# Performance work log

Hardware: AMD Instinct MI355X
Metric: run time of the kernel (lower is better)

## Reference

```python
import jax, jax.numpy as jnp
import numpy as np

N = 10000
E = 160000
F_IN = 2000
HID = 128
NC = 5


def setup_inputs() -> dict:
    key = jax.random.key(0)
    ks = jax.random.split(key, 16)
    s = 0.05
    nrm = lambda k, shape: jax.random.normal(k, shape, jnp.float32) * s
    return {
        "x": jax.random.normal(ks[0], (N, F_IN), jnp.float32),
        "edge_index": jax.random.randint(ks[1], (2, E), 0, N),
        # GATConv 1: in=F_IN, out=HID, heads=6, concat=False
        "W_gat1": nrm(ks[2], (F_IN, 6 * HID)), "a_src1": nrm(ks[3], (6, HID)),
        "a_dst1": nrm(ks[4], (6, HID)), "b_gat1": jnp.zeros(HID, jnp.float32),
        # GCNConv 1
        "W_gcn1": nrm(ks[5], (HID, HID)), "b_gcn1": jnp.zeros(HID, jnp.float32),
        # GATConv 2: heads=4
        "W_gat2": nrm(ks[6], (HID, 4 * HID)), "a_src2": nrm(ks[7], (4, HID)),
        "a_dst2": nrm(ks[8], (4, HID)), "b_gat2": jnp.zeros(HID, jnp.float32),
        # GCNConv 2: out=HID//2
        "W_gcn2": nrm(ks[9], (HID, HID // 2)), "b_gcn2": jnp.zeros(HID // 2, jnp.float32),
        # skip projection / fusion
        "W_skip": nrm(ks[10], (F_IN, HID // 2)), "b_skip": jnp.zeros(HID // 2, jnp.float32),
        "W_fuse": nrm(ks[11], (HID + HID // 2, HID // 2)), "b_fuse": jnp.zeros(HID // 2, jnp.float32),
        # classifier MLP
        "W_c1": nrm(ks[12], (HID // 2, HID // 4)), "b_c1": jnp.zeros(HID // 4, jnp.float32),
        "W_c2": nrm(ks[13], (HID // 4, HID // 8)), "b_c2": jnp.zeros(HID // 8, jnp.float32),
        "W_c3": nrm(ks[14], (HID // 8, NC)), "b_c3": jnp.zeros(NC, jnp.float32),
        # LayerNorms
        "g1": jnp.ones(HID, jnp.float32), "be1": jnp.zeros(HID, jnp.float32),
        "g2": jnp.ones(HID, jnp.float32), "be2": jnp.zeros(HID, jnp.float32),
        "g3": jnp.ones(HID // 2, jnp.float32), "be3": jnp.zeros(HID // 2, jnp.float32),
    }


def layer_norm(x, g, b, eps=1e-5):
    mu = jnp.mean(x, axis=-1, keepdims=True)
    var = jnp.var(x, axis=-1, keepdims=True)
    return (x - mu) * jax.lax.rsqrt(var + eps) * g + b


def gat_conv(x, src, dst, W, a_src, a_dst, b, n):
    # PyG GATConv with concat=False (head-mean). Eval mode -> no attn dropout.
    H, C = a_src.shape
    h = (x @ W).reshape(-1, H, C)                      # [N,H,C]
    alpha = (h * a_src).sum(-1)[src] + (h * a_dst).sum(-1)[dst]  # [E,H]
    alpha = jax.nn.leaky_relu(alpha, 0.2)
    m = jax.ops.segment_max(alpha, dst, num_segments=n)
    e = jnp.exp(alpha - m[dst])
    w = e / jax.ops.segment_sum(e, dst, num_segments=n)[dst]     # segment softmax over incoming edges
    out = jax.ops.segment_sum(h[src] * w[:, :, None], dst, num_segments=n)  # [N,H,C]
    return out.mean(axis=1) + b


def gcn_conv(x, src, dst, W, b, n):
    deg = jax.ops.segment_sum(jnp.ones_like(dst, x.dtype), dst, num_segments=n)
    dinv = jnp.where(deg > 0, deg ** -0.5, 0.0)
    msg = (x @ W)[src] * (dinv[src] * dinv[dst])[:, None]
    return jax.ops.segment_sum(msg, dst, num_segments=n) + b


def reference(x, edge_index, W_gat1, a_src1, a_dst1, b_gat1, W_gcn1, b_gcn1,
              W_gat2, a_src2, a_dst2, b_gat2, W_gcn2, b_gcn2,
              W_skip, b_skip, W_fuse, b_fuse, W_c1, b_c1, W_c2, b_c2, W_c3, b_c3,
              g1, be1, g2, be2, g3, be3):
    n = x.shape[0]
    loop = jnp.arange(n, dtype=edge_index.dtype)
    src = jnp.concatenate([edge_index[0], loop])  # add_self_loops
    dst = jnp.concatenate([edge_index[1], loop])

    x1_gat = jax.nn.relu(layer_norm(gat_conv(x, src, dst, W_gat1, a_src1, a_dst1, b_gat1, n), g1, be1))
    x1_gcn = jax.nn.relu(gcn_conv(x1_gat, src, dst, W_gcn1, b_gcn1, n))
    x2_gat = jax.nn.relu(layer_norm(gat_conv(x1_gcn, src, dst, W_gat2, a_src2, a_dst2, b_gat2, n), g2, be2))
    x2_gcn = jax.nn.relu(gcn_conv(x2_gat, src, dst, W_gcn2, b_gcn2, n))

    skip = jax.nn.relu(x @ W_skip + b_skip)
    fused = jax.nn.relu(jnp.concatenate([x1_gcn, x2_gcn], axis=1) @ W_fuse + b_fuse)
    final = layer_norm(fused + skip, g3, be3)

    h = jax.nn.relu(final @ W_c1 + b_c1)
    h = jax.nn.relu(h @ W_c2 + b_c2)
    return h @ W_c3 + b_c3
```

## Files before the change

### kernel.cpp

```cpp
#include <hip/hip_runtime.h>
#include <cstdint>
#include <cstddef>

#define NN 10000
#define NE 160000
#define ET (NE + NN)
#define FIN 2000
#define MPAD 10112
#define KPAD 2048
#define NPAD 896

typedef __bf16 bf16x8 __attribute__((ext_vector_type(8)));
typedef __bf16 bf16x4 __attribute__((ext_vector_type(4)));
typedef float  f32x4  __attribute__((ext_vector_type(4)));

#define GLL(src, dst) __builtin_amdgcn_global_load_lds( \
    (const __attribute__((address_space(1))) void*)(src), \
    (__attribute__((address_space(3))) void*)(dst), 16, 0, 0)

__device__ __forceinline__ void edge_sd(const int* ei, int e, int& s, int& d) {
    if (e < NE) { s = ei[e]; d = ei[NE + e]; }
    else        { s = e - NE; d = e - NE; }
}

__global__ void scan_kernel(const int* deg, int* rowstart, float* dinv) {
    __shared__ int partial[256];
    const int T = 256;
    int chunk = (NN + T - 1) / T;
    int t = threadIdx.x;
    int begin = t * chunk;
    int end = begin + chunk; if (end > NN) end = NN;
    int s = 0;
    for (int i = begin; i < end && i >= begin; i++) s += deg[i];
    partial[t] = s;
    __syncthreads();
    if (t == 0) {
        int run = 0;
        for (int i = 0; i < T; i++) { int v = partial[i]; partial[i] = run; run += v; }
    }
    __syncthreads();
    int run = partial[t];
    for (int i = begin; i < end && i >= begin; i++) {
        rowstart[i] = run; run += deg[i];
        int dg = deg[i];
        dinv[i] = dg > 0 ? rsqrtf((float)dg) : 0.f;
    }
    if (end == NN && begin <= NN) rowstart[NN] = run;
}

__global__ void scatter_kernel(const int* ei, const int* rowstart, int* cursor,
                               int* csr_src) {
    int e = blockIdx.x * blockDim.x + threadIdx.x;
    if (e >= ET) return;
    int s, d; edge_sd(ei, e, s, d);
    int pos = atomicAdd(&cursor[d], 1);
    csr_src[rowstart[d] + pos] = s;
}

#define NBX (158 * 32)
#define NW1 (NPAD * KPAD / 8)
#define NWT (NW1 + 512 * 128 / 8)
#define NWT2 (NWT + 2048 + 1024)
#define WBLK ((NWT2 + 255) / 256)
#define EB 665
__global__ void conv_kernel(const float* __restrict__ x, __bf16* __restrict__ xb,
                            const float* __restrict__ Wg, const float* __restrict__ Ws,
                            const float* __restrict__ W2,
                            const float* __restrict__ Wg1, const float* __restrict__ Wg2,
                            __bf16* __restrict__ wt, __bf16* __restrict__ w2t,
                            __bf16* __restrict__ wgcn1s, __bf16* __restrict__ wgcn2s,
                            const int* __restrict__ ei, int* __restrict__ deg) {
    __shared__ __bf16 slab[4096];
    int bid = blockIdx.x;
    int tid = threadIdx.x;
    if (bid < NBX) {
        int rt = bid >> 5, ks = bid & 31;
        int r = tid >> 2;
        int row = rt * 64 + r;
        int c0 = (tid & 3) * 16;
        int kbase = ks * 64;
#pragma unroll
        for (int j = 0; j < 4; j++) {
            int kl = c0 + j * 4;
            int k = kbase + kl;
            bf16x4 o;
            if (row < NN && k + 3 < FIN) {
                float4 v = *(const float4*)(x + (size_t)row * FIN + k);
                o[0] = (__bf16)v.x; o[1] = (__bf16)v.y;
                o[2] = (__bf16)v.z; o[3] = (__bf16)v.w;
            } else {
                o[0] = o[1] = o[2] = o[3] = (__bf16)0.f;
            }
            int p = kl >> 3, off = kl & 7;
            *(bf16x4*)(slab + (p * 64 + r) * 8 + off) = o;
        }
        __syncthreads();
        size_t base = (size_t)(rt * 32 + ks) * 512;
#pragma unroll
        for (int i = 0; i < 2; i++) {
            int c = i * 256 + tid;
            *(bf16x8*)(xb + (base + c) * 8) = *(const bf16x8*)(slab + c * 8);
        }
    } else if (bid < NBX + WBLK) {
        int g = (bid - NBX) * 256 + tid;
        if (g < NW1) {
            int r = g & 127, p = (g >> 7) & 7, ks = (g >> 10) & 31, ct = g >> 15;
            int n = ct * 128 + r;
            int k0 = ks * 64 + p * 8;
            bf16x8 o;
#pragma unroll
            for (int j = 0; j < 8; j++) {
                int k = k0 + j;
                float v = 0.f;
                if (k < FIN) {
                    if (n < 768)      v = Wg[(size_t)k * 768 + n];
                    else if (n < 832) v = Ws[(size_t)k * 64 + (n - 768)];
                }
                o[j] = (__bf16)v;
            }
            *(bf16x8*)(wt + (size_t)g * 8) = o;
        } else if (g < NWT) {
            int g2 = g - NW1;
            int c = g2 & 2047;
            int ct = g2 >> 11;
            int p = c >> 7, r = c & 127;
            int n = ct * 128 + r;
            int k0 = p * 8;
            bf16x8 o;
#pragma unroll
            for (int j = 0; j < 8; j++)
                o[j] = (__bf16)W2[(size_t)(k0 + j) * 512 + n];
            *(bf16x8*)(w2t + (size_t)g2 * 8) = o;
        } else if (g < NWT + 2048) {
            int g3 = g - NWT;
            int p = g3 >> 7, r = g3 & 127;
            bf16x8 o;
#pragma unroll
            for (int j = 0; j < 8; j++)
                o[j] = (__bf16)Wg1[(size_t)(p * 8 + j) * 128 + r];
            *(bf16x8*)(wgcn1s + (size_t)g3 * 8) = o;
        } else if (g < NWT2) {
            int g4 = g - NWT - 2048;
            int p = g4 >> 6, r = g4 & 63;
            bf16x8 o;
#pragma unroll
            for (int j = 0; j < 8; j++)
                o[j] = (__bf16)Wg2[(size_t)(p * 8 + j) * 64 + r];
            *(bf16x8*)(wgcn2s + (size_t)g4 * 8) = o;
        }
    } else {
        int e = (bid - NBX - WBLK) * 256 + tid;
        if (e < ET) {
            int s, d; edge_sd(ei, e, s, d);
            atomicAdd(&deg[d], 1);
        }
    }
}

__global__ __launch_bounds__(256)
void mfma_gemm1_kernel(const __bf16* __restrict__ xb, const __bf16* __restrict__ wt,
                       const float* __restrict__ a_src1, const float* __restrict__ a_dst1,
                       __bf16* __restrict__ h1b, float* __restrict__ skippre,
                       float* __restrict__ asrc, float* __restrict__ adst) {
    __shared__ __bf16 As[4096];
    __shared__ __bf16 Bs[8192];
    __shared__ float sA[64], sD[64];
    __shared__ float asd[256];
    int b = blockIdx.x;
    int xcd = b & 7, j = b >> 3;
    int jq = j / 7;
    int rt = xcd + 8 * jq;
    int ct = j - 7 * jq;
    if (rt >= MPAD / 64) return;
    const int bi = rt * 64;
    const int bn = ct * 128;

    const int tid = threadIdx.x;
    const int lane = tid & 63;
    const int w = tid >> 6;
    const int wm = w >> 1, wn = w & 1;
    const int q = lane >> 4, m16 = lane & 15;

    if (tid < 64) { sA[tid] = 0.f; sD[tid] = 0.f; }
    if (ct < 6) {
        if (tid < 128) asd[tid] = a_src1[ct * 128 + tid];
        else           asd[tid] = a_dst1[ct * 128 + (tid - 128)];
    }

    f32x4 acc[2][4] = {};

    for (int ks = 0; ks < KPAD / 64; ks++) {
        const size_t slabA = (size_t)(rt * 32 + ks) * 512;
        const size_t slabB = (size_t)(ct * 32 + ks) * 1024;
#pragma unroll
        for (int i = 0; i < 2; i++) {
            int seg = i * 4 + w;
            GLL(xb + (slabA + seg * 64 + lane) * 8, As + seg * 512);
        }
#pragma unroll
        for (int i = 0; i < 4; i++) {
            int seg = i * 4 + w;
            GLL(wt + (slabB + seg * 64 + lane) * 8, Bs + seg * 512);
        }
        __syncthreads();

#pragma unroll
        for (int kk = 0; kk < 2; kk++) {
            const int pb = kk * 4 + q;
            bf16x8 af[2], bfr[4];
#pragma unroll
            for (int mt = 0; mt < 2; mt++)
                af[mt] = *(const bf16x8*)(As + (pb * 64 + wm * 32 + mt * 16 + m16) * 8);
#pragma unroll
            for (int nt = 0; nt < 4; nt++)
                bfr[nt] = *(const bf16x8*)(Bs + (pb * 128 + wn * 64 + nt * 16 + m16) * 8);
#pragma unroll
            for (int mt = 0; mt < 2; mt++)
#pragma unroll
                for (int nt = 0; nt < 4; nt++)
                    acc[mt][nt] = __builtin_amdgcn_mfma_f32_16x16x32_bf16(af[mt], bfr[nt], acc[mt][nt], 0, 0, 0);
        }
        __syncthreads();
    }

#pragma unroll
    for (int mt = 0; mt < 2; mt++) {
#pragma unroll
        for (int r = 0; r < 4; r++) {
            int rowl = wm * 32 + mt * 16 + q * 4 + r;
            int row = bi + rowl;
            float ps = 0.f, pd = 0.f;
#pragma unroll
            for (int nt = 0; nt < 4; nt++) {
                int coll = wn * 64 + nt * 16 + m16;
                int col = bn + coll;
                float v = acc[mt][nt][r];
                if (ct < 6) { ps += v * asd[coll]; pd += v * asd[128 + coll]; }
                if (row < NN) {
                    if (col < 768)      h1b[(size_t)row * 768 + col] = (__bf16)v;
                    else if (col < 832) skippre[(size_t)row * 64 + (col - 768)] = v;
                }
            }
            if (ct < 6) {
#pragma unroll
                for (int off = 1; off < 16; off <<= 1) {
                    ps += __shfl_xor(ps, off);
                    pd += __shfl_xor(pd, off);
                }
                if (m16 == 0) { atomicAdd(&sA[rowl], ps); atomicAdd(&sD[rowl], pd); }
            }
        }
    }
    if (ct < 6) {
        __syncthreads();
        if (tid < 64) {
            int row = bi + tid;
            if (row < NN) { asrc[row * 6 + ct] = sA[tid]; adst[row * 6 + ct] = sD[tid]; }
        }
    }
}

__global__ __launch_bounds__(256)
void mfma_gemm2_kernel(const __bf16* __restrict__ A, const __bf16* __restrict__ B,
                       const float* __restrict__ a_src2, const float* __restrict__ a_dst2,
                       __bf16* __restrict__ h2b,
                       float* __restrict__ asrc, float* __restrict__ adst) {
    __shared__ __bf16 As[4096];
    __shared__ __bf16 Bs[8192];
    __shared__ float sA[64], sD[64];
    __shared__ float asd[256];
    const int rt = blockIdx.y, ct = blockIdx.x;
    const int bi = rt * 64, bn = ct * 128;
    const int tid = threadIdx.x, lane = tid & 63, w = tid >> 6;
    const int wm = w >> 1, wn = w & 1;
    const int q = lane >> 4, m16 = lane & 15;

    if (tid < 64) { sA[tid] = 0.f; sD[tid] = 0.f; }
    if (tid < 128) asd[tid] = a_src2[ct * 128 + tid];
    else           asd[tid] = a_dst2[ct * 128 + (tid - 128)];

    f32x4 acc[2][4] = {};

    for (int ks = 0; ks < 2; ks++) {
        const size_t slabA = (size_t)rt * 1024 + ks * 512;
        const size_t slabB = (size_t)ct * 2048 + ks * 1024;
#pragma unroll
        for (int i = 0; i < 2; i++) {
            int seg = i * 4 + w;
            GLL(A + (slabA + seg * 64 + lane) * 8, As + seg * 512);
        }
#pragma unroll
        for (int i = 0; i < 4; i++) {
            int seg = i * 4 + w;
            GLL(B + (slabB + seg * 64 + lane) * 8, Bs + seg * 512);
        }
        __syncthreads();

#pragma unroll
        for (int kk = 0; kk < 2; kk++) {
            const int pb = kk * 4 + q;
            bf16x8 af[2], bfr[4];
#pragma unroll
            for (int mt = 0; mt < 2; mt++)
                af[mt] = *(const bf16x8*)(As + (pb * 64 + wm * 32 + mt * 16 + m16) * 8);
#pragma unroll
            for (int nt = 0; nt < 4; nt++)
                bfr[nt] = *(const bf16x8*)(Bs + (pb * 128 + wn * 64 + nt * 16 + m16) * 8);
#pragma unroll
            for (int mt = 0; mt < 2; mt++)
#pragma unroll
                for (int nt = 0; nt < 4; nt++)
                    acc[mt][nt] = __builtin_amdgcn_mfma_f32_16x16x32_bf16(af[mt], bfr[nt], acc[mt][nt], 0, 0, 0);
        }
        __syncthreads();
    }

#pragma unroll
    for (int mt = 0; mt < 2; mt++) {
#pragma unroll
        for (int r = 0; r < 4; r++) {
            int rowl = wm * 32 + mt * 16 + q * 4 + r;
            int row = bi + rowl;
            float ps = 0.f, pd = 0.f;
#pragma unroll
            for (int nt = 0; nt < 4; nt++) {
                int coll = wn * 64 + nt * 16 + m16;
                float v = acc[mt][nt][r];
                ps += v * asd[coll]; pd += v * asd[128 + coll];
                if (row < NN) h2b[(size_t)row * 512 + bn + coll] = (__bf16)v;
            }
#pragma unroll
            for (int off = 1; off < 16; off <<= 1) {
                ps += __shfl_xor(ps, off);
                pd += __shfl_xor(pd, off);
            }
            if (m16 == 0) { atomicAdd(&sA[rowl], ps); atomicAdd(&sD[rowl], pd); }
        }
    }
    __syncthreads();
    if (tid < 64) {
        int row = bi + tid;
        if (row < NN) { asrc[row * 4 + ct] = sA[tid]; adst[row * 4 + ct] = sD[tid]; }
    }
}

template<int NT>
__global__ __launch_bounds__(256)
void mfma_gcn_kernel(const __bf16* __restrict__ A, const __bf16* __restrict__ B,
                     __bf16* __restrict__ Cb) {
    __shared__ __bf16 As[4096];
    __shared__ __bf16 Bs[NT * 64];
    const int rt = blockIdx.x;
    const int bi = rt * 64;
    const int tid = threadIdx.x, lane = tid & 63, w = tid >> 6;
    const int q = lane >> 4, m16 = lane & 15;
    constexpr int MT = (NT == 128) ? 2 : 1;
    constexpr int MSPAN = (NT == 128) ? 32 : 16;
    const int wm = (NT == 128) ? (w >> 1) : w;
    const int wn = (NT == 128) ? (w & 1) : 0;

    f32x4 acc[MT][4] = {};

    for (int ks = 0; ks < 2; ks++) {
        const size_t slabA = (size_t)rt * 1024 + ks * 512;
        const size_t slabB = (size_t)ks * (NT * 8);
#pragma unroll
        for (int i = 0; i < 2; i++) {
            int seg = i * 4 + w;
            GLL(A + (slabA + seg * 64 + lane) * 8, As + seg * 512);
        }
#pragma unroll
        for (int i = 0; i < NT / 32; i++) {
            int seg = i * 4 + w;
            GLL(B + (slabB + (size_t)seg * 64 + lane) * 8, Bs + seg * 512);
        }
        __syncthreads();

#pragma unroll
        for (int kk = 0; kk < 2; kk++) {
            const int pb = kk * 4 + q;
            bf16x8 af[MT], bfr[4];
#pragma unroll
            for (int mt = 0; mt < MT; mt++)
                af[mt] = *(const bf16x8*)(As + (pb * 64 + wm * MSPAN + mt * 16 + m16) * 8);
#pragma unroll
            for (int nt = 0; nt < 4; nt++)
                bfr[nt] = *(const bf16x8*)(Bs + (pb * NT + wn * 64 + nt * 16 + m16) * 8);
#pragma unroll
            for (int mt = 0; mt < MT; mt++)
#pragma unroll
                for (int nt = 0; nt < 4; nt++)
                    acc[mt][nt] = __builtin_amdgcn_mfma_f32_16x16x32_bf16(af[mt], bfr[nt], acc[mt][nt], 0, 0, 0);
        }
        __syncthreads();
    }

#pragma unroll
    for (int mt = 0; mt < MT; mt++) {
#pragma unroll
        for (int r = 0; r < 4; r++) {
            int row = bi + wm * MSPAN + mt * 16 + q * 4 + r;
            if (row >= NN) continue;
#pragma unroll
            for (int nt = 0; nt < 4; nt++) {
                int col = wn * 64 + nt * 16 + m16;
                Cb[(size_t)row * NT + col] = (__bf16)acc[mt][nt][r];
            }
        }
    }
}

template<int H>
__global__ void gat_agg_kernel(const __bf16* __restrict__ hb,
                               const float* __restrict__ asrc,
                               const float* __restrict__ adst,
                               const int* __restrict__ rowstart,
                               const int* __restrict__ csr_src,
                               const float* __restrict__ bias,
                               const float* __restrict__ gamma,
                               const float* __restrict__ beta,
                               __bf16* __restrict__ outs) {
    constexpr int CH = H * 128;
    constexpr int CAP = 128;
    int n = blockIdx.x;
    int t = threadIdx.x;
    int w = t >> 6, l = t & 63;
    __shared__ float invden[H];
    __shared__ float denw[4][H];
    __shared__ int   srcs[CAP];
    __shared__ float evs[CAP * H];
    __shared__ float sm[4 * CH];
    __shared__ float red[8];

    int s0 = rowstart[n];
    int deg = rowstart[n + 1] - s0;
    float adst_n = (l < H) ? adst[n * H + l] : 0.f;

    float dloc = 0.f;
    for (int idx = w; idx < deg; idx += 4) {
        int src = csr_src[s0 + idx];
        if (idx < CAP && l == 0) srcs[idx] = src;
        if (l < H) {
            float al = asrc[src * H + l] + adst_n;
            al = al >= 0.f ? al : 0.2f * al;
            float ev = __expf(al);
            dloc += ev;
            if (idx < CAP) evs[idx * H + l] = ev;
        }
    }
    if (l < H) denw[w][l] = dloc;
    __syncthreads();
    if (t < H) invden[t] = 1.f / (denw[0][t] + denw[1][t] + denw[2][t] + denw[3][t]);
    __syncthreads();

    constexpr int NA = (H == 6) ? 12 : 8;
    float acc[NA] = {};
    const int h0 = l >> 4;
    const int h1i = 4 + (l >> 5);
    int degc = deg < CAP ? deg : CAP;
    int idx = w;
    for (; idx + 4 < degc; idx += 8) {
        int src0 = srcs[idx], src1 = srcs[idx + 4];
        float w00 = evs[idx * H + h0];
        float w10 = evs[(idx + 4) * H + h0];
        const __bf16* hp0 = hb + (size_t)src0 * CH;
        const __bf16* hp1 = hb + (size_t)src1 * CH;
        bf16x8 g00 = *(const bf16x8*)(hp0 + l * 8);
        bf16x8 g10 = *(const bf16x8*)(hp1 + l * 8);
#pragma unroll
        for (int jj = 0; jj < 8; jj++)
            acc[jj] += (float)g00[jj] * w00 + (float)g10[jj] * w10;
        if (H == 6) {
            float w01 = evs[idx * H + h1i];
            float w11 = evs[(idx + 4) * H + h1i];
            bf16x4 g01 = *(const bf16x4*)(hp0 + 512 + l * 4);
            bf16x4 g11 = *(const bf16x4*)(hp1 + 512 + l * 4);
#pragma unroll
            for (int jj = 0; jj < 4; jj++)
                acc[8 + jj] += (float)g01[jj] * w01 + (float)g11[jj] * w11;
        }
    }
    if (idx < degc) {
        int src = srcs[idx];
        float w0 = evs[idx * H + h0];
        const __bf16* hp = hb + (size_t)src * CH;
        bf16x8 hv = *(const bf16x8*)(hp + l * 8);
#pragma unroll
        for (int jj = 0; jj < 8; jj++) acc[jj] += (float)hv[jj] * w0;
        if (H == 6) {
            float w1 = evs[idx * H + h1i];
            bf16x4 hv1 = *(const bf16x4*)(hp + 512 + l * 4);
#pragma unroll
            for (int jj = 0; jj < 4; jj++) acc[8 + jj] += (float)hv1[jj] * w1;
        }
    }
    for (int i2 = CAP + w; i2 < deg; i2 += 4) {
        int src = csr_src[s0 + i2];
        float ev = 0.f;
        if (l < H) {
            float al = asrc[src * H + l] + adst_n;
            al = al >= 0.f ? al : 0.2f * al;
            ev = __expf(al);
        }
        const __bf16* hp = hb + (size_t)src * CH;
        float wgt = __shfl(ev, h0);
        bf16x8 hv = *(const bf16x8*)(hp + l * 8);
#pragma unroll
        for (int jj = 0; jj < 8; jj++) acc[jj] += (float)hv[jj] * wgt;
        if (H == 6) {
            float wg1 = __shfl(ev, h1i);
            bf16x4 hv1 = *(const bf16x4*)(hp + 512 + l * 4);
#pragma unroll
            for (int jj = 0; jj < 4; jj++) acc[8 + jj] += (float)hv1[jj] * wg1;
        }
    }

    *(f32x4*)(sm + w * CH + l * 8)     = *(f32x4*)(acc);
    *(f32x4*)(sm + w * CH + l * 8 + 4) = *(f32x4*)(acc + 4);
    if (H == 6)
        *(f32x4*)(sm + w * CH + 512 + l * 4) = *(f32x4*)(acc + 8);
    __syncthreads();

    float v = 0.f;
    if (t < 128) {
#pragma unroll
        for (int hh = 0; hh < H; hh++) {
            float hsum = 0.f;
#pragma unroll
            for (int ww = 0; ww < 4; ww++) hsum += sm[ww * CH + hh * 128 + t];
            v += hsum * invden[hh];
        }
        v = v * (1.f / H) + bias[t];
    }
    float sv = (t < 128) ? v : 0.f;
    float sq = (t < 128) ? v * v : 0.f;
#pragma unroll
    for (int off = 32; off; off >>= 1) {
        sv += __shfl_down(sv, off);
        sq += __shfl_down(sq, off);
    }
    if ((t & 63) == 0) { red[w * 2] = sv; red[w * 2 + 1] = sq; }
    __syncthreads();
    float tot = red[0] + red[2] + red[4] + red[6];
    float tsq = red[1] + red[3] + red[5] + red[7];
    float mu = tot * (1.f / 128.f);
    float var = tsq * (1.f / 128.f) - mu * mu;
    float r = rsqrtf(var + 1e-5f);
    if (t < 128) {
        float o = fmaxf((v - mu) * r * gamma[t] + beta[t], 0.f);
        int rt2 = n >> 6, rr = n & 63, pp = t >> 3, off2 = t & 7;
        outs[((size_t)(rt2 * 16 + pp) * 64 + rr) * 8 + off2] = (__bf16)o;
    }
}

__global__ void gcn_agg_kernel(const __bf16* __restrict__ y, int C,
                               const float* __restrict__ dinv,
                               const int* __restrict__ rowstart,
                               const int* __restrict__ csr_src,
                               const float* __restrict__ bias,
                               float* __restrict__ out, int ldo, int coloff,
                               __bf16* __restrict__ bout) {
    int n = blockIdx.x;
    int t = threadIdx.x;
    float acc = 0.f;
    int s0 = rowstart[n], s1 = rowstart[n + 1];
    for (int s = s0; s < s1; s++) {
        int src = csr_src[s];
        acc += (float)y[(size_t)src * C + t] * dinv[src];
    }
    float v = fmaxf(acc * dinv[n] + bias[t], 0.f);
    out[(size_t)n * ldo + coloff + t] = v;
    if (bout) {
        int rt = n >> 6, r = n & 63, p = t >> 3, off = t & 7;
        bout[((size_t)(rt * 16 + p) * 64 + r) * 8 + off] = (__bf16)v;
    }
}

__global__ __launch_bounds__(256)
void fuse_final_kernel(const float* __restrict__ cat,
                       const float* __restrict__ skippre,
                       const float* __restrict__ Wf, const float* __restrict__ bfz,
                       const float* __restrict__ b_skip,
                       const float* __restrict__ g3, const float* __restrict__ be3,
                       const float* __restrict__ Wc1, const float* __restrict__ bc1,
                       const float* __restrict__ Wc2, const float* __restrict__ bc2,
                       const float* __restrict__ Wc3, const float* __restrict__ bc3,
                       float* __restrict__ out) {
    __shared__ float WfS[192 * 64];
    __shared__ float catS[4][196];
    __shared__ float fS[4][64], h1S[4][32], h2S[4][16];
    int tid = threadIdx.x;
    int w = tid >> 6, l = tid & 63;
#pragma unroll
    for (int i = 0; i < 12; i++) {
        int idx = (i * 256 + tid) * 4;
        *(f32x4*)(WfS + idx) = *(const f32x4*)(Wf + idx);
    }
    int n = blockIdx.x * 4 + w;
    bool act = n < NN;
    float sk = 0.f;
    if (act) {
        catS[w][l]       = cat[(size_t)n * 192 + l];
        catS[w][64 + l]  = cat[(size_t)n * 192 + 64 + l];
        catS[w][128 + l] = cat[(size_t)n * 192 + 128 + l];
        sk = fmaxf(skippre[(size_t)n * 64 + l] + b_skip[l], 0.f);
    }
    __syncthreads();

    float fu = bfz[l];
#pragma unroll 4
    for (int k = 0; k < 192; k++)
        fu += catS[w][k] * WfS[k * 64 + l];
    float v = fmaxf(fu, 0.f) + sk;

    float sv = v, sq = v * v;
#pragma unroll
    for (int off = 32; off; off >>= 1) {
        sv += __shfl_xor(sv, off);
        sq += __shfl_xor(sq, off);
    }
    float mu = sv * (1.f / 64.f);
    float var = sq * (1.f / 64.f) - mu * mu;
    float r = rsqrtf(var + 1e-5f);
    fS[w][l] = (v - mu) * r * g3[l] + be3[l];
    __syncthreads();
    if (l < 32) {
        float a = bc1[l];
        for (int i = 0; i < 64; i++) a += fS[w][i] * Wc1[i * 32 + l];
        h1S[w][l] = fmaxf(a, 0.f);
    }
    __syncthreads();
    if (l < 16) {
        float a = bc2[l];
        for (int i = 0; i < 32; i++) a += h1S[w][i] * Wc2[i * 16 + l];
        h2S[w][l] = fmaxf(a, 0.f);
    }
    __syncthreads();
    if (l < 5 && act) {
        float a = bc3[l];
        for (int i = 0; i < 16; i++) a += h2S[w][i] * Wc3[i * 5 + l];
        out[(size_t)n * 5 + l] = a;
    }
}

extern "C" void kernel_launch(void* const* d_in, const int* in_sizes, int n_in,
                              void* d_out, int out_size, void* d_ws, size_t ws_size,
                              hipStream_t stream) {
    const float* x      = (const float*)d_in[0];
    const int*   ei     = (const int*)d_in[1];
    const float* W_gat1 = (const float*)d_in[2];
    const float* a_src1 = (const float*)d_in[3];
    const float* a_dst1 = (const float*)d_in[4];
    const float* b_gat1 = (const float*)d_in[5];
    const float* W_gcn1 = (const float*)d_in[6];
    const float* b_gcn1 = (const float*)d_in[7];
    const float* W_gat2 = (const float*)d_in[8];
    const float* a_src2 = (const float*)d_in[9];
    const float* a_dst2 = (const float*)d_in[10];
    const float* b_gat2 = (const float*)d_in[11];
    const float* W_gcn2 = (const float*)d_in[12];
    const float* b_gcn2 = (const float*)d_in[13];
    const float* W_skip = (const float*)d_in[14];
    const float* b_skip = (const float*)d_in[15];
    const float* W_fuse = (const float*)d_in[16];
    const float* b_fuse = (const float*)d_in[17];
    const float* W_c1   = (const float*)d_in[18];
    const float* b_c1   = (const float*)d_in[19];
    const float* W_c2   = (const float*)d_in[20];
    const float* b_c2   = (const float*)d_in[21];
    const float* W_c3   = (const float*)d_in[22];
    const float* b_c3   = (const float*)d_in[23];
    const float* g1     = (const float*)d_in[24];
    const float* be1    = (const float*)d_in[25];
    const float* g2     = (const float*)d_in[26];
    const float* be2    = (const float*)d_in[27];
    const float* g3     = (const float*)d_in[28];
    const float* be3    = (const float*)d_in[29];
    float* out = (float*)d_out;

    char* p = (char*)d_ws;
    auto alloc = [&](size_t bytes) {
        char* r = p; p += (bytes + 255) & ~(size_t)255; return r;
    };
    __bf16* xb      = (__bf16*)alloc((size_t)MPAD * KPAD * 2);
    __bf16* wt      = (__bf16*)alloc((size_t)NPAD * KPAD * 2);
    __bf16* w2t     = (__bf16*)alloc((size_t)512 * 128 * 2);
    __bf16* wgcn1s  = (__bf16*)alloc((size_t)128 * 128 * 2);
    __bf16* wgcn2s  = (__bf16*)alloc((size_t)64 * 128 * 2);
    __bf16* h1b     = (__bf16*)alloc((size_t)NN * 768 * 2);
    __bf16* h2b     = (__bf16*)alloc((size_t)NN * 512 * 2);
    __bf16* ybufb   = (__bf16*)alloc((size_t)NN * 128 * 2);
    __bf16* x1gatb  = (__bf16*)alloc((size_t)3 * MPAD * 128 * 2);
    __bf16* x1gcnb  = x1gatb + (size_t)MPAD * 128;
    __bf16* x2gatb  = x1gcnb + (size_t)MPAD * 128;
    float* asrc     = (float*)alloc((size_t)NN * 6 * 4);
    float* adst     = (float*)alloc((size_t)NN * 6 * 4);
    int*   deg      = (int*)  alloc((size_t)2 * NN * 4);
    int*   cursor   = deg + NN;
    float* dinv     = (float*)alloc((size_t)NN * 4);
    int*   rowst    = (int*)  alloc((size_t)(NN + 1) * 4);
    int*   csrc     = (int*)  alloc((size_t)ET * 4);
    float* cat      = (float*)alloc((size_t)NN * 192 * 4);
    float* skippre  = (float*)alloc((size_t)NN * 64 * 4);

    hipMemsetAsync(deg, 0, (size_t)2 * NN * 4, stream);
    hipMemsetAsync(x1gatb, 0, (size_t)3 * MPAD * 128 * 2, stream);

    conv_kernel<<<NBX + WBLK + EB, 256, 0, stream>>>(
        x, xb, W_gat1, W_skip, W_gat2, W_gcn1, W_gcn2,
        wt, w2t, wgcn1s, wgcn2s, ei, deg);

    scan_kernel   <<<1, 256, 0, stream>>>(deg, rowst, dinv);
    scatter_kernel<<<EB, 256, 0, stream>>>(ei, rowst, cursor, csrc);

    mfma_gemm1_kernel<<<1120, 256, 0, stream>>>(xb, wt, a_src1, a_dst1,
                                                h1b, skippre, asrc, adst);

    gat_agg_kernel<6><<<NN, 256, 0, stream>>>(h1b, asrc, adst, rowst, csrc,
                                              b_gat1, g1, be1, x1gatb);
    mfma_gcn_kernel<128><<<MPAD / 64, 256, 0, stream>>>(x1gatb, wgcn1s, ybufb);
    gcn_agg_kernel<<<NN, 128, 0, stream>>>(ybufb, 128, dinv, rowst, csrc,
                                           b_gcn1, cat, 192, 0, x1gcnb);
    mfma_gemm2_kernel<<<dim3(4, MPAD / 64), 256, 0, stream>>>(
        x1gcnb, w2t, a_src2, a_dst2, h2b, asrc, adst);
    gat_agg_kernel<4><<<NN, 256, 0, stream>>>(h2b, asrc, adst, rowst, csrc,
                                              b_gat2, g2, be2, x2gatb);
    mfma_gcn_kernel<64><<<MPAD / 64, 256, 0, stream>>>(x2gatb, wgcn2s, ybufb);
    gcn_agg_kernel<<<NN, 64, 0, stream>>>(ybufb, 64, dinv, rowst, csrc,
                                          b_gcn2, cat, 192, 128, nullptr);
    fuse_final_kernel<<<(NN + 3) / 4, 256, 0, stream>>>(
        cat, skippre, W_fuse, b_fuse, b_skip, g3, be3,
        W_c1, b_c1, W_c2, b_c2, W_c3, b_c3, out);
}
```

Baseline: 469.1 us.

## Fold CSR scatter into GEMM1 launch, split GCN edges across groups, amortize fuse weights

The CSR scatter kernel is removed and its work runs as extra trailing blocks of the first MFMA GEMM launch, which saves one launch and lets the scatter overlap with the GEMM. The GCN aggregation kernel is templated on channel count and uses 256 threads, so several thread groups split each node's edge list and combine partial sums through shared memory. The fuse/final kernel processes 16 nodes per block instead of 4, so the 48KB fusion weight matrix is loaded into shared memory fewer times. The costs are extra barriers and a shared-memory reduction in the aggregation, and fewer blocks in the fuse kernel.

After: 532.2 us. 13.5% more time.

```diff
diff --git a/kernel.cpp b/kernel.cpp
--- a/kernel.cpp
+++ b/kernel.cpp
@@ -46,15 +46,6 @@
         dinv[i] = dg > 0 ? rsqrtf((float)dg) : 0.f;
     }
     if (end == NN && begin <= NN) rowstart[NN] = run;
-}
-
-__global__ void scatter_kernel(const int* ei, const int* rowstart, int* cursor,
-                               int* csr_src) {
-    int e = blockIdx.x * blockDim.x + threadIdx.x;
-    if (e >= ET) return;
-    int s, d; edge_sd(ei, e, s, d);
-    int pos = atomicAdd(&cursor[d], 1);
-    csr_src[rowstart[d] + pos] = s;
 }
 
 #define NBX (158 * 32)
@@ -157,16 +148,28 @@
     }
 }
 
+#define G1BLK 1120
 __global__ __launch_bounds__(256)
 void mfma_gemm1_kernel(const __bf16* __restrict__ xb, const __bf16* __restrict__ wt,
                        const float* __restrict__ a_src1, const float* __restrict__ a_dst1,
                        __bf16* __restrict__ h1b, float* __restrict__ skippre,
-                       float* __restrict__ asrc, float* __restrict__ adst) {
+                       float* __restrict__ asrc, float* __restrict__ adst,
+                       const int* __restrict__ ei, const int* __restrict__ rowstart,
+                       int* __restrict__ cursor, int* __restrict__ csr_src) {
     __shared__ __bf16 As[4096];
     __shared__ __bf16 Bs[8192];
     __shared__ float sA[64], sD[64];
     __shared__ float asd[256];
     int b = blockIdx.x;
+    if (b >= G1BLK) {
+        int e = (b - G1BLK) * 256 + threadIdx.x;
+        if (e < ET) {
+            int s, d; edge_sd(ei, e, s, d);
+            int pos = atomicAdd(&cursor[d], 1);
+            csr_src[rowstart[d] + pos] = s;
+        }
+        return;
+    }
     int xcd = b & 7, j = b >> 3;
     int jq = j / 7;
     int rt = xcd + 8 * jq;
@@ -553,26 +556,36 @@
     }
 }
 
-__global__ void gcn_agg_kernel(const __bf16* __restrict__ y, int C,
+template<int C>
+__global__ void gcn_agg_kernel(const __bf16* __restrict__ y,
                                const float* __restrict__ dinv,
                                const int* __restrict__ rowstart,
                                const int* __restrict__ csr_src,
                                const float* __restrict__ bias,
                                float* __restrict__ out, int ldo, int coloff,
                                __bf16* __restrict__ bout) {
+    constexpr int G = 256 / C;
     int n = blockIdx.x;
     int t = threadIdx.x;
+    int g = t / C, ch = t % C;
+    __shared__ float part[256];
     float acc = 0.f;
     int s0 = rowstart[n], s1 = rowstart[n + 1];
-    for (int s = s0; s < s1; s++) {
+    for (int s = s0 + g; s < s1; s += G) {
         int src = csr_src[s];
-        acc += (float)y[(size_t)src * C + t] * dinv[src];
-    }
-    float v = fmaxf(acc * dinv[n] + bias[t], 0.f);
-    out[(size_t)n * ldo + coloff + t] = v;
-    if (bout) {
-        int rt = n >> 6, r = n & 63, p = t >> 3, off = t & 7;
-        bout[((size_t)(rt * 16 + p) * 64 + r) * 8 + off] = (__bf16)v;
+        acc += (float)y[(size_t)src * C + ch] * dinv[src];
+    }
+    part[t] = acc;
+    __syncthreads();
+    if (g == 0) {
+#pragma unroll
+        for (int i = 1; i < G; i++) acc += part[i * C + ch];
+        float v = fmaxf(acc * dinv[n] + bias[ch], 0.f);
+        out[(size_t)n * ldo + coloff + ch] = v;
+        if (bout) {
+            int rt = n >> 6, r = n & 63, p = ch >> 3, off = ch & 7;
+            bout[((size_t)(rt * 16 + p) * 64 + r) * 8 + off] = (__bf16)v;
+        }
     }
 }
 
@@ -596,50 +609,55 @@
         int idx = (i * 256 + tid) * 4;
         *(f32x4*)(WfS + idx) = *(const f32x4*)(Wf + idx);
     }
-    int n = blockIdx.x * 4 + w;
-    bool act = n < NN;
-    float sk = 0.f;
-    if (act) {
-        catS[w][l]       = cat[(size_t)n * 192 + l];
-        catS[w][64 + l]  = cat[(size_t)n * 192 + 64 + l];
-        catS[w][128 + l] = cat[(size_t)n * 192 + 128 + l];
-        sk = fmaxf(skippre[(size_t)n * 64 + l] + b_skip[l], 0.f);
-    }
-    __syncthreads();
-
-    float fu = bfz[l];
+    __syncthreads();
+
+    for (int it = 0; it < 4; it++) {
+        int n = blockIdx.x * 16 + it * 4 + w;
+        bool act = n < NN;
+        float sk = 0.f;
+        if (act) {
+            catS[w][l]       = cat[(size_t)n * 192 + l];
+            catS[w][64 + l]  = cat[(size_t)n * 192 + 64 + l];
+            catS[w][128 + l] = cat[(size_t)n * 192 + 128 + l];
+            sk = fmaxf(skippre[(size_t)n * 64 + l] + b_skip[l], 0.f);
+        }
+        __syncthreads();
+
+        float fu = bfz[l];
 #pragma unroll 4
-    for (int k = 0; k < 192; k++)
-        fu += catS[w][k] * WfS[k * 64 + l];
-    float v = fmaxf(fu, 0.f) + sk;
-
-    float sv = v, sq = v * v;
-#pragma unroll
-    for (int off = 32; off; off >>= 1) {
-        sv += __shfl_xor(sv, off);
-        sq += __shfl_xor(sq, off);
-    }
-    float mu = sv * (1.f / 64.f);
-    float var = sq * (1.f / 64.f) - mu * mu;
-    float r = rsqrtf(var + 1e-5f);
-    fS[w][l] = (v - mu) * r * g3[l] + be3[l];
-    __syncthreads();
-    if (l < 32) {
-        float a = bc1[l];
-        for (int i = 0; i < 64; i++) a += fS[w][i] * Wc1[i * 32 + l];
-        h1S[w][l] = fmaxf(a, 0.f);
-    }
-    __syncthreads();
-    if (l < 16) {
-        float a = bc2[l];
-        for (int i = 0; i < 32; i++) a += h1S[w][i] * Wc2[i * 16 + l];
-        h2S[w][l] = fmaxf(a, 0.f);
-    }
-    __syncthreads();
-    if (l < 5 && act) {
-        float a = bc3[l];
-        for (int i = 0; i < 16; i++) a += h2S[w][i] * Wc3[i * 5 + l];
-        out[(size_t)n * 5 + l] = a;
+        for (int k = 0; k < 192; k++)
+            fu += catS[w][k] * WfS[k * 64 + l];
+        float v = fmaxf(fu, 0.f) + sk;
+
+        float sv = v, sq = v * v;
+#pragma unroll
+        for (int off = 32; off; off >>= 1) {
+            sv += __shfl_xor(sv, off);
+            sq += __shfl_xor(sq, off);
+        }
+        float mu = sv * (1.f / 64.f);
+        float var = sq * (1.f / 64.f) - mu * mu;
+        float r = rsqrtf(var + 1e-5f);
+        fS[w][l] = (v - mu) * r * g3[l] + be3[l];
+        __syncthreads();
+        if (l < 32) {
+            float a = bc1[l];
+            for (int i = 0; i < 64; i++) a += fS[w][i] * Wc1[i * 32 + l];
+            h1S[w][l] = fmaxf(a, 0.f);
+        }
+        __syncthreads();
+        if (l < 16) {
+            float a = bc2[l];
+            for (int i = 0; i < 32; i++) a += h1S[w][i] * Wc2[i * 16 + l];
+            h2S[w][l] = fmaxf(a, 0.f);
+        }
+        __syncthreads();
+        if (l < 5 && act) {
+            float a = bc3[l];
+            for (int i = 0; i < 16; i++) a += h2S[w][i] * Wc3[i * 5 + l];
+            out[(size_t)n * 5 + l] = a;
+        }
+        __syncthreads();
     }
 }
 
@@ -710,25 +728,25 @@
         x, xb, W_gat1, W_skip, W_gat2, W_gcn1, W_gcn2,
         wt, w2t, wgcn1s, wgcn2s, ei, deg);
 
-    scan_kernel   <<<1, 256, 0, stream>>>(deg, rowst, dinv);
-    scatter_kernel<<<EB, 256, 0, stream>>>(ei, rowst, cursor, csrc);
-
-    mfma_gemm1_kernel<<<1120, 256, 0, stream>>>(xb, wt, a_src1, a_dst1,
-                                                h1b, skippre, asrc, adst);
+    scan_kernel<<<1, 256, 0, stream>>>(deg, rowst, dinv);
+
+    mfma_gemm1_kernel<<<G1BLK + EB, 256, 0, stream>>>(
+        xb, wt, a_src1, a_dst1, h1b, skippre, asrc, adst,
+        ei, rowst, cursor, csrc);
 
     gat_agg_kernel<6><<<NN, 256, 0, stream>>>(h1b, asrc, adst, rowst, csrc,
                                               b_gat1, g1, be1, x1gatb);
     mfma_gcn_kernel<128><<<MPAD / 64, 256, 0, stream>>>(x1gatb, wgcn1s, ybufb);
-    gcn_agg_kernel<<<NN, 128, 0, stream>>>(ybufb, 128, dinv, rowst, csrc,
-                                           b_gcn1, cat, 192, 0, x1gcnb);
+    gcn_agg_kernel<128><<<NN, 256, 0, stream>>>(ybufb, dinv, rowst, csrc,
+                                                b_gcn1, cat, 192, 0, x1gcnb);
     mfma_gemm2_kernel<<<dim3(4, MPAD / 64), 256, 0, stream>>>(
         x1gcnb, w2t, a_src2, a_dst2, h2b, asrc, adst);
     gat_agg_kernel<4><<<NN, 256, 0, stream>>>(h2b, asrc, adst, rowst, csrc,
                                               b_gat2, g2, be2, x2gatb);
     mfma_gcn_kernel<64><<<MPAD / 64, 256, 0, stream>>>(x2gatb, wgcn2s, ybufb);
-    gcn_agg_kernel<<<NN, 64, 0, stream>>>(ybufb, 64, dinv, rowst, csrc,
-                                          b_gcn2, cat, 192, 128, nullptr);
-    fuse_final_kernel<<<(NN + 3) / 4, 256, 0, stream>>>(
+    gcn_agg_kernel<64><<<NN, 256, 0, stream>>>(ybufb, dinv, rowst, csrc,
+                                               b_gcn2, cat, 192, 128, nullptr);
+    fuse_final_kernel<<<(NN + 15) / 16, 256, 0, stream>>>(
         cat, skippre, W_fuse, b_fuse, b_skip, g3, be3,
         W_c1, b_c1, W_c2, b_c2, W_c3, b_c3, out);
 }
```
